# Performance work log

Hardware: AMD Instinct MI355X
Metric: run time of the kernel (lower is better)

The kernel has to match this reference:

```python
import jax, jax.numpy as jnp
import numpy as np

INPUT_DIM = 128
HIDDEN_DIM = 256
TOP_K = 512
M = 8192
N = 8192


def setup_inputs() -> dict:
    key = jax.random.key(0)
    ks = jax.random.split(key, 10)
    s_in = 1.0 / np.sqrt(INPUT_DIM)
    s_h = 1.0 / np.sqrt(HIDDEN_DIM)
    return {
        "desc0": jax.random.normal(ks[0], (1, M, INPUT_DIM), jnp.float32),
        "desc1": jax.random.normal(ks[1], (1, N, INPUT_DIM), jnp.float32),
        # mlpc0: Linear(in,h) -> ReLU -> Linear(h,h); weights stored [in,out]
        "W0a": jax.random.uniform(ks[2], (INPUT_DIM, HIDDEN_DIM), jnp.float32, -s_in, s_in),
        "b0a": jax.random.uniform(ks[3], (HIDDEN_DIM,), jnp.float32, -s_in, s_in),
        "W0b": jax.random.uniform(ks[4], (HIDDEN_DIM, HIDDEN_DIM), jnp.float32, -s_h, s_h),
        "b0b": jax.random.uniform(ks[5], (HIDDEN_DIM,), jnp.float32, -s_h, s_h),
        "W1a": jax.random.uniform(ks[6], (INPUT_DIM, HIDDEN_DIM), jnp.float32, -s_in, s_in),
        "b1a": jax.random.uniform(ks[7], (HIDDEN_DIM,), jnp.float32, -s_in, s_in),
        "W1b": jax.random.uniform(ks[8], (HIDDEN_DIM, HIDDEN_DIM), jnp.float32, -s_h, s_h),
        "b1b": jax.random.uniform(ks[9], (HIDDEN_DIM,), jnp.float32, -s_h, s_h),
    }


def _mlp(x, Wa, ba, Wb, bb):
    h = jax.nn.relu(x @ Wa + ba)
    return h @ Wb + bb


def reference(desc0, desc1, W0a, b0a, W0b, b0b, W1a, b1a, W1b, b1b):
    mdesc0 = _mlp(desc0, W0a, b0a, W0b, b0b)  # [1, M, H]
    mdesc1 = _mlp(desc1, W1a, b1a, W1b, b1b)  # [1, N, H]
    sim = jnp.einsum("bmd,bnd->bmn", mdesc0, mdesc1)  # [1, M, N]
    flat = sim[0].reshape(-1)
    _, top_idx = jax.lax.top_k(flat, TOP_K)
    n = sim.shape[2]
    rows = top_idx // n
    cols = top_idx % n
    top_k_indices_2d = jnp.stack([rows, cols], axis=1)  # [TOP_K, 2]
    return top_k_indices_2d, sim
```

## Files before the change

### kernel.cpp

```cpp
#include <hip/hip_runtime.h>
#include <stdint.h>

#define H_DIM 256
#define NCOL 8192
#define TOPK 512
#define CAND_CAP 8192

typedef unsigned short u16;
typedef __attribute__((ext_vector_type(8))) __bf16 bf16x8;
typedef __attribute__((ext_vector_type(4))) float f32x4;
typedef unsigned __attribute__((address_space(3))) lds_u32;
typedef const unsigned __attribute__((address_space(1))) glb_u32;

__device__ __forceinline__ unsigned fkey(float f) {
  unsigned u = __float_as_uint(f);
  unsigned m = (unsigned)((int)u >> 31) | 0x80000000u;
  return u ^ m;
}

__device__ __forceinline__ u16 f2bf_rne(float f) {
  unsigned u = __float_as_uint(f);
  return (u16)((u + 0x7fffu + ((u >> 16) & 1u)) >> 16);
}

__device__ __forceinline__ float bf2f(u16 h) {
  return __uint_as_float(((unsigned)h) << 16);
}

__global__ __launch_bounds__(256) void mlp_fused(
    const float* __restrict__ X0, const float* __restrict__ W0a,
    const float* __restrict__ b0a, const float* __restrict__ W0b,
    const float* __restrict__ b0b, float* __restrict__ Y0,
    u16* __restrict__ h0, u16* __restrict__ l0,
    const float* __restrict__ X1, const float* __restrict__ W1a,
    const float* __restrict__ b1a, const float* __restrict__ W1b,
    const float* __restrict__ b1b, float* __restrict__ Y1,
    u16* __restrict__ h1, u16* __restrict__ l1,
    unsigned* __restrict__ ghist, unsigned* __restrict__ counter) {
  __shared__ float Xs[16 * 128];
  __shared__ float Hs[16 * 256];
  const int t = threadIdx.x;
  if (blockIdx.x == 0) {
    for (int i = t; i < 4096; i += 256) ghist[i] = 0;
    if (t == 0) *counter = 0;
  }
  const int half = blockIdx.x >> 9;
  const float* X = half ? X1 : X0;
  const float* Wa = half ? W1a : W0a;
  const float* ba = half ? b1a : b0a;
  const float* Wb = half ? W1b : W0b;
  const float* bb_ = half ? b1b : b0b;
  float* Y = half ? Y1 : Y0;
  u16* hi = half ? h1 : h0;
  u16* lo = half ? l1 : l0;
  const int row0 = (blockIdx.x & 511) * 16;

  for (int f = t; f < 512; f += 256) {
    *(float4*)(Xs + f * 4) = *(const float4*)(X + (size_t)row0 * 128 + f * 4);
  }
  __syncthreads();
  const int cg = (t & 63) * 4;
  const int rg = (t >> 6) * 4;

  {
    float acc[4][4];
#pragma unroll
    for (int r = 0; r < 4; r++)
#pragma unroll
      for (int c = 0; c < 4; c++) acc[r][c] = 0.f;
    for (int d = 0; d < 128; d += 4) {
      float4 w0 = *(const float4*)(Wa + (d + 0) * H_DIM + cg);
      float4 w1 = *(const float4*)(Wa + (d + 1) * H_DIM + cg);
      float4 w2 = *(const float4*)(Wa + (d + 2) * H_DIM + cg);
      float4 w3 = *(const float4*)(Wa + (d + 3) * H_DIM + cg);
#pragma unroll
      for (int r = 0; r < 4; r++) {
        float4 x = *(const float4*)(Xs + (rg + r) * 128 + d);
#pragma unroll
        for (int c = 0; c < 4; c++) {
          float a = acc[r][c];
          a = fmaf(x.x, ((const float*)&w0)[c], a);
          a = fmaf(x.y, ((const float*)&w1)[c], a);
          a = fmaf(x.z, ((const float*)&w2)[c], a);
          a = fmaf(x.w, ((const float*)&w3)[c], a);
          acc[r][c] = a;
        }
      }
    }
    const float4 bv = *(const float4*)(ba + cg);
#pragma unroll
    for (int r = 0; r < 4; r++) {
      float4 v;
      v.x = fmaxf(acc[r][0] + bv.x, 0.f);
      v.y = fmaxf(acc[r][1] + bv.y, 0.f);
      v.z = fmaxf(acc[r][2] + bv.z, 0.f);
      v.w = fmaxf(acc[r][3] + bv.w, 0.f);
      *(float4*)(Hs + (rg + r) * 256 + cg) = v;
    }
  }
  __syncthreads();

  {
    float acc[4][4];
#pragma unroll
    for (int r = 0; r < 4; r++)
#pragma unroll
      for (int c = 0; c < 4; c++) acc[r][c] = 0.f;
    for (int d = 0; d < 256; d += 4) {
      float4 w0 = *(const float4*)(Wb + (d + 0) * H_DIM + cg);
      float4 w1 = *(const float4*)(Wb + (d + 1) * H_DIM + cg);
      float4 w2 = *(const float4*)(Wb + (d + 2) * H_DIM + cg);
      float4 w3 = *(const float4*)(Wb + (d + 3) * H_DIM + cg);
#pragma unroll
      for (int r = 0; r < 4; r++) {
        float4 x = *(const float4*)(Hs + (rg + r) * 256 + d);
#pragma unroll
        for (int c = 0; c < 4; c++) {
          float a = acc[r][c];
          a = fmaf(x.x, ((const float*)&w0)[c], a);
          a = fmaf(x.y, ((const float*)&w1)[c], a);
          a = fmaf(x.z, ((const float*)&w2)[c], a);
          a = fmaf(x.w, ((const float*)&w3)[c], a);
          acc[r][c] = a;
        }
      }
    }
    const float4 bv = *(const float4*)(bb_ + cg);
#pragma unroll
    for (int r = 0; r < 4; r++) {
      float4 v;
      v.x = acc[r][0] + bv.x;
      v.y = acc[r][1] + bv.y;
      v.z = acc[r][2] + bv.z;
      v.w = acc[r][3] + bv.w;
      const size_t grow = (size_t)(row0 + rg + r);
      *(float4*)(Y + grow * H_DIM + cg) = v;
      ushort4 hv, lv;
      hv.x = f2bf_rne(v.x); lv.x = f2bf_rne(v.x - bf2f(hv.x));
      hv.y = f2bf_rne(v.y); lv.y = f2bf_rne(v.y - bf2f(hv.y));
      hv.z = f2bf_rne(v.z); lv.z = f2bf_rne(v.z - bf2f(hv.z));
      hv.w = f2bf_rne(v.w); lv.w = f2bf_rne(v.w - bf2f(hv.w));
      *(ushort4*)(hi + grow * H_DIM + cg) = hv;
      *(ushort4*)(lo + grow * H_DIM + cg) = lv;
    }
  }
}

__global__ __launch_bounds__(512, 2) void gemm_sim_mfma(const u16* __restrict__ Ah,
                                                        const u16* __restrict__ Al,
                                                        const u16* __restrict__ Bh,
                                                        const u16* __restrict__ Bl,
                                                        float* __restrict__ C,
                                                        unsigned* __restrict__ ghist) {
  __shared__ __align__(16) char SB[131072];
  const int t = threadIdx.x;
  const int wave = t >> 6, lane = t & 63;
  const int wm = wave >> 2, wn = wave & 3;
  const int bid = blockIdx.x;
  const int swz = (bid & 7) * 128 + (bid >> 3);
  const int m0 = (swz >> 5) * 256, n0 = (swz & 31) * 256;

  f32x4 acc[8][4];
#pragma unroll
  for (int i = 0; i < 8; i++)
#pragma unroll
    for (int j = 0; j < 4; j++) acc[i][j] = (f32x4){0.f, 0.f, 0.f, 0.f};

  const int srow8 = t >> 3;
  const int sA = (t & 7) ^ (srow8 & 7);
  const u16* pAsrc = (sA < 4) ? Ah : Al;
  const u16* pBsrc = (sA < 4) ? Bh : Bl;
  const int scolE = (sA & 3) * 8;
  const int lrow = lane & 15;
  const int kq16 = (lane >> 4) << 4;
  const int asz = (lrow & 7) << 4;
  const int cH = kq16 ^ asz;
  const int cL = (64 + kq16) ^ asz;

  auto STAGE = [&](int bsel, int tt) {
    const int kofs = tt * 32;
    char* base = SB + bsel * 65536;
    const size_t ar = (size_t)(m0 + srow8) * H_DIM + kofs + scolE;
    const size_t br = (size_t)(n0 + srow8) * H_DIM + kofs + scolE;
#pragma unroll
    for (int i = 0; i < 4; i++)
      __builtin_amdgcn_global_load_lds((glb_u32*)(pAsrc + ar + (size_t)i * 64 * H_DIM),
                                       (lds_u32*)(base + i * 8192 + wave * 1024), 16, 0, 0);
#pragma unroll
    for (int i = 0; i < 4; i++)
      __builtin_amdgcn_global_load_lds((glb_u32*)(pBsrc + br + (size_t)i * 64 * H_DIM),
                                       (lds_u32*)(base + 32768 + i * 8192 + wave * 1024), 16, 0, 0);
  };

  STAGE(0, 0);
  for (int tt = 0; tt < 8; ++tt) {
    if (tt < 7) {
      STAGE((tt + 1) & 1, tt + 1);
      asm volatile("s_waitcnt vmcnt(8)" ::: "memory");
    } else {
      asm volatile("s_waitcnt vmcnt(0)" ::: "memory");
    }
    __builtin_amdgcn_s_barrier();
    asm volatile("" ::: "memory");
    const char* bb = SB + (tt & 1) * 65536;
    const char* bA = bb + (wm * 128 + lrow) * 128;
    const char* bB = bb + 32768 + (wn * 64 + lrow) * 128;

    bf16x8 aH[8], bH[4];
#pragma unroll
    for (int fm = 0; fm < 8; fm++) aH[fm] = *(const bf16x8*)(bA + fm * 2048 + cH);
#pragma unroll
    for (int fn = 0; fn < 4; fn++) bH[fn] = *(const bf16x8*)(bB + fn * 2048 + cH);
    __builtin_amdgcn_s_setprio(1);
#pragma unroll
    for (int fm = 0; fm < 8; fm++)
#pragma unroll
      for (int fn = 0; fn < 4; fn++)
        acc[fm][fn] = __builtin_amdgcn_mfma_f32_16x16x32_bf16(aH[fm], bH[fn], acc[fm][fn], 0, 0, 0);
    __builtin_amdgcn_s_setprio(0);
    __builtin_amdgcn_s_barrier();

    {
      bf16x8 bL[4];
#pragma unroll
      for (int fn = 0; fn < 4; fn++) bL[fn] = *(const bf16x8*)(bB + fn * 2048 + cL);
      __builtin_amdgcn_s_setprio(1);
#pragma unroll
      for (int fm = 0; fm < 8; fm++)
#pragma unroll
        for (int fn = 0; fn < 4; fn++)
          acc[fm][fn] = __builtin_amdgcn_mfma_f32_16x16x32_bf16(aH[fm], bL[fn], acc[fm][fn], 0, 0, 0);
      __builtin_amdgcn_s_setprio(0);
    }
    __builtin_amdgcn_s_barrier();

    {
      bf16x8 aL[8];
#pragma unroll
      for (int fm = 0; fm < 8; fm++) aL[fm] = *(const bf16x8*)(bA + fm * 2048 + cL);
      __builtin_amdgcn_s_setprio(1);
#pragma unroll
      for (int fm = 0; fm < 8; fm++)
#pragma unroll
        for (int fn = 0; fn < 4; fn++)
          acc[fm][fn] = __builtin_amdgcn_mfma_f32_16x16x32_bf16(aL[fm], bH[fn], acc[fm][fn], 0, 0, 0);
      __builtin_amdgcn_s_setprio(0);
    }
    __builtin_amdgcn_s_barrier();
    asm volatile("" ::: "memory");
  }

  unsigned* hist = (unsigned*)SB;
  float* Ct = (float*)(SB + 16384);
  for (int i = t; i < 4096; i += 512) hist[i] = 0;
  __syncthreads();
#pragma unroll
  for (int ch = 0; ch < 4; ++ch) {
    if (wm == (ch >> 1)) {
      const int fmb = (ch & 1) * 4;
#pragma unroll
      for (int fi = 0; fi < 4; fi++)
#pragma unroll
        for (int fn = 0; fn < 4; fn++)
#pragma unroll
          for (int q = 0; q < 4; q++)
            Ct[(fi * 16 + (lane >> 4) * 4 + q) * 260 + wn * 64 + fn * 16 + lrow] =
                acc[fmb + fi][fn][q];
    }
    __syncthreads();
#pragma unroll
    for (int u = 0; u < 8; ++u) {
      const int idx = t + u * 512;
      const int row = idx >> 6, c4 = idx & 63;
      float4 v = *(const float4*)(Ct + row * 260 + c4 * 4);
      *(float4*)(C + (size_t)(m0 + ch * 64 + row) * NCOL + n0 + c4 * 4) = v;
      atomicAdd(&hist[fkey(v.x) >> 20], 1u);
      atomicAdd(&hist[fkey(v.y) >> 20], 1u);
      atomicAdd(&hist[fkey(v.z) >> 20], 1u);
      atomicAdd(&hist[fkey(v.w) >> 20], 1u);
    }
    __syncthreads();
  }
  for (int bq = t; bq < 4096; bq += 512) {
    unsigned cc = hist[bq];
    if (cc) atomicAdd(&ghist[bq], cc);
  }
}

__device__ __forceinline__ void cand_push(unsigned kapprox, unsigned thr_m, unsigned idx,
                                          const float* __restrict__ m0f,
                                          const float* __restrict__ m1f,
                                          unsigned long long* __restrict__ cand,
                                          unsigned* __restrict__ counter) {
  if (kapprox >= thr_m) {
    const unsigned row = idx >> 13;
    const unsigned col = idx & 8191u;
    const float4* a4 = (const float4*)(m0f + (size_t)row * H_DIM);
    const float4* b4 = (const float4*)(m1f + (size_t)col * H_DIM);
    float v = 0.f;
#pragma unroll 8
    for (int k = 0; k < H_DIM / 4; k++) {
      float4 a = a4[k], b = b4[k];
      v = fmaf(a.x, b.x, v);
      v = fmaf(a.y, b.y, v);
      v = fmaf(a.z, b.z, v);
      v = fmaf(a.w, b.w, v);
    }
    unsigned p = atomicAdd(counter, 1u);
    if (p < CAND_CAP)
      cand[p] = ((unsigned long long)fkey(v) << 32) |
                (unsigned long long)(0xFFFFFFFFu - idx);
  }
}

__global__ __launch_bounds__(256) void collect(const float* __restrict__ sim,
                                               const unsigned* __restrict__ ghist,
                                               const float* __restrict__ m0f,
                                               const float* __restrict__ m1f,
                                               unsigned long long* __restrict__ cand,
                                               unsigned* __restrict__ counter) {
  __shared__ unsigned part[256];
  __shared__ unsigned thr_sh;
  const int t = threadIdx.x;
  {
    unsigned s = 0;
#pragma unroll
    for (int b = 0; b < 16; b++) s += ghist[t * 16 + b];
    part[t] = s;
    __syncthreads();
    for (int off = 1; off < 256; off <<= 1) {
      unsigned v = part[t] + ((t + off < 256) ? part[t + off] : 0u);
      __syncthreads();
      part[t] = v;
      __syncthreads();
    }
    if (part[t] >= TOPK && (t == 255 || part[t + 1] < TOPK)) {
      unsigned cum = (t == 255) ? 0u : part[t + 1];
      int bsel = t * 16;
      for (int b = t * 16 + 15; b >= t * 16; --b) {
        cum += ghist[b];
        if (cum >= TOPK) { bsel = b; break; }
      }
      thr_sh = (unsigned)bsel << 20;
    }
    __syncthreads();
  }
  const unsigned thr = thr_sh;
  const unsigned thr_m = thr > 4096u ? thr - 4096u : 0u;
  const int stride = gridDim.x * blockDim.x;
  const int total4 = (NCOL * NCOL) / 4;
  const float4* s4 = (const float4*)sim;
  for (int i = blockIdx.x * blockDim.x + threadIdx.x; i < total4; i += stride) {
    float4 v = s4[i];
    unsigned base = (unsigned)i * 4u;
    cand_push(fkey(v.x), thr_m, base + 0u, m0f, m1f, cand, counter);
    cand_push(fkey(v.y), thr_m, base + 1u, m0f, m1f, cand, counter);
    cand_push(fkey(v.z), thr_m, base + 2u, m0f, m1f, cand, counter);
    cand_push(fkey(v.w), thr_m, base + 3u, m0f, m1f, cand, counter);
  }
}

__global__ __launch_bounds__(1024) void sort_topk(const unsigned long long* __restrict__ cand,
                                                  const unsigned* __restrict__ counter,
                                                  float* __restrict__ out) {
  __shared__ unsigned long long top[TOPK];
  __shared__ unsigned wred[16];
  __shared__ unsigned long long pfx_sh;
  __shared__ unsigned cnt_sh;
  const int t = threadIdx.x;
  const int n = (int)min(*counter, (unsigned)CAND_CAP);
  unsigned long long e[CAND_CAP / 1024];
#pragma unroll
  for (int u = 0; u < CAND_CAP / 1024; ++u) {
    const int i = t + u * 1024;
    e[u] = (i < n) ? cand[i] : 0ULL;
  }
  if (t == 0) cnt_sh = 0;
  __syncthreads();
  unsigned long long pfx = 0;
  for (int b = 63; b >= 0; --b) {
    const unsigned long long q = pfx | (1ULL << b);
    unsigned c = 0;
#pragma unroll
    for (int u = 0; u < CAND_CAP / 1024; ++u) c += (e[u] >= q) ? 1u : 0u;
#pragma unroll
    for (int off = 32; off; off >>= 1) c += __shfl_down(c, off, 64);
    if ((t & 63) == 0) wred[t >> 6] = c;
    __syncthreads();
    if (t == 0) {
      unsigned tot = 0;
#pragma unroll
      for (int w = 0; w < 16; ++w) tot += wred[w];
      pfx_sh = (tot >= TOPK) ? q : pfx;
    }
    __syncthreads();
    pfx = pfx_sh;
  }
#pragma unroll
  for (int u = 0; u < CAND_CAP / 1024; ++u) {
    if (e[u] >= pfx) {
      unsigned p = atomicAdd(&cnt_sh, 1u);
      if (p < TOPK) top[p] = e[u];
    }
  }
  __syncthreads();
  for (int k = 2; k <= TOPK; k <<= 1) {
    for (int j = k >> 1; j > 0; j >>= 1) {
      if (t < TOPK) {
        const int l = t ^ j;
        if (l > t) {
          const bool desc = ((t & k) == 0);
          unsigned long long a = top[t], b2 = top[l];
          if (desc ? (a < b2) : (a > b2)) { top[t] = b2; top[l] = a; }
        }
      }
      __syncthreads();
    }
  }
  if (t < TOPK) {
    const unsigned idx = 0xFFFFFFFFu - (unsigned)(top[t] & 0xFFFFFFFFull);
    out[t * 2 + 0] = (float)(idx >> 13);
    out[t * 2 + 1] = (float)(idx & 8191u);
  }
}

extern "C" void kernel_launch(void* const* d_in, const int* in_sizes, int n_in,
                              void* d_out, int out_size, void* d_ws, size_t ws_size,
                              hipStream_t stream) {
  const float* desc0 = (const float*)d_in[0];
  const float* desc1 = (const float*)d_in[1];
  const float* W0a = (const float*)d_in[2];
  const float* b0a = (const float*)d_in[3];
  const float* W0b = (const float*)d_in[4];
  const float* b0b = (const float*)d_in[5];
  const float* W1a = (const float*)d_in[6];
  const float* b1a = (const float*)d_in[7];
  const float* W1b = (const float*)d_in[8];
  const float* b1b = (const float*)d_in[9];

  char* ws = (char*)d_ws;
  unsigned* ghist = (unsigned*)ws;
  unsigned* counter = (unsigned*)(ws + 16384);
  unsigned long long* cand = (unsigned long long*)(ws + 16448);
  float* mdesc0f = (float*)(ws + 131072);
  float* mdesc1f = mdesc0f + 8192 * 256;
  u16* Ahh = (u16*)(mdesc1f + 8192 * 256);
  u16* All = Ahh + 8192 * 256;
  u16* Bhh = All + 8192 * 256;
  u16* Bll = Bhh + 8192 * 256;

  float* outf = (float*)d_out;
  float* sim = outf + TOPK * 2;

  mlp_fused<<<1024, 256, 0, stream>>>(
      desc0, W0a, b0a, W0b, b0b, mdesc0f, Ahh, All,
      desc1, W1a, b1a, W1b, b1b, mdesc1f, Bhh, Bll, ghist, counter);

  gemm_sim_mfma<<<1024, 512, 0, stream>>>(Ahh, All, Bhh, Bll, sim, ghist);
  collect<<<4096, 256, 0, stream>>>(sim, ghist, mdesc0f, mdesc1f, cand, counter);
  sort_topk<<<1, 1024, 0, stream>>>(cand, counter, outf);
}
```

Before: 544.9 us.

## Record per-64x64 tile maxima in GEMM and rescan only qualifying tiles

The GEMM epilogue now reduces each wave's 64x64 sub-tile to a max key and writes it to a tile-max table. The collect step is split into a single-block scan that computes the histogram threshold and builds a worklist of tiles whose max passes it, plus a gather kernel that re-reads only those tiles from sim. This avoids re-reading the full 256 MB similarity matrix just to find candidates. It adds a small serial kernel launch, some extra reduction work in the GEMM epilogue, and a worklist whose size depends on the data.

```diff
diff --git a/kernel.cpp b/kernel.cpp
--- a/kernel.cpp
+++ b/kernel.cpp
@@ -36,13 +36,14 @@
     const float* __restrict__ b1a, const float* __restrict__ W1b,
     const float* __restrict__ b1b, float* __restrict__ Y1,
     u16* __restrict__ h1, u16* __restrict__ l1,
-    unsigned* __restrict__ ghist, unsigned* __restrict__ counter) {
+    unsigned* __restrict__ ghist, unsigned* __restrict__ counter,
+    unsigned* __restrict__ nwork) {
   __shared__ float Xs[16 * 128];
   __shared__ float Hs[16 * 256];
   const int t = threadIdx.x;
   if (blockIdx.x == 0) {
     for (int i = t; i < 4096; i += 256) ghist[i] = 0;
-    if (t == 0) *counter = 0;
+    if (t == 0) { *counter = 0; *nwork = 0; }
   }
   const int half = blockIdx.x >> 9;
   const float* X = half ? X1 : X0;
@@ -151,7 +152,8 @@
                                                         const u16* __restrict__ Bh,
                                                         const u16* __restrict__ Bl,
                                                         float* __restrict__ C,
-                                                        unsigned* __restrict__ ghist) {
+                                                        unsigned* __restrict__ ghist,
+                                                        unsigned* __restrict__ tilemax) {
   __shared__ __align__(16) char SB[131072];
   const int t = threadIdx.x;
   const int wave = t >> 6, lane = t & 63;
@@ -250,6 +252,29 @@
     asm volatile("" ::: "memory");
   }
 
+  {
+    float mx0 = -3.4e38f, mx1 = -3.4e38f;
+#pragma unroll
+    for (int fm = 0; fm < 4; fm++)
+#pragma unroll
+      for (int fn = 0; fn < 4; fn++)
+#pragma unroll
+        for (int q = 0; q < 4; q++) {
+          mx0 = fmaxf(mx0, acc[fm][fn][q]);
+          mx1 = fmaxf(mx1, acc[fm + 4][fn][q]);
+        }
+#pragma unroll
+    for (int off = 1; off < 64; off <<= 1) {
+      mx0 = fmaxf(mx0, __shfl_xor(mx0, off, 64));
+      mx1 = fmaxf(mx1, __shfl_xor(mx1, off, 64));
+    }
+    if (lane == 0) {
+      const int str = (m0 >> 6) + wm * 2, stc = (n0 >> 6) + wn;
+      tilemax[str * 128 + stc] = fkey(mx0);
+      tilemax[(str + 1) * 128 + stc] = fkey(mx1);
+    }
+  }
+
   unsigned* hist = (unsigned*)SB;
   float* Ct = (float*)(SB + 16384);
   for (int i = t; i < 4096; i += 512) hist[i] = 0;
@@ -284,6 +309,46 @@
   for (int bq = t; bq < 4096; bq += 512) {
     unsigned cc = hist[bq];
     if (cc) atomicAdd(&ghist[bq], cc);
+  }
+}
+
+__global__ __launch_bounds__(256) void collect_scan(const unsigned* __restrict__ ghist,
+                                                    const unsigned* __restrict__ tilemax,
+                                                    unsigned* __restrict__ thrm_out,
+                                                    int* __restrict__ worklist,
+                                                    unsigned* __restrict__ nwork) {
+  __shared__ unsigned part[256];
+  __shared__ unsigned thr_sh;
+  const int t = threadIdx.x;
+  unsigned s = 0;
+#pragma unroll
+  for (int b = 0; b < 16; b++) s += ghist[t * 16 + b];
+  part[t] = s;
+  __syncthreads();
+  for (int off = 1; off < 256; off <<= 1) {
+    unsigned v = part[t] + ((t + off < 256) ? part[t + off] : 0u);
+    __syncthreads();
+    part[t] = v;
+    __syncthreads();
+  }
+  if (part[t] >= TOPK && (t == 255 || part[t + 1] < TOPK)) {
+    unsigned cum = (t == 255) ? 0u : part[t + 1];
+    int bsel = t * 16;
+    for (int b = t * 16 + 15; b >= t * 16; --b) {
+      cum += ghist[b];
+      if (cum >= TOPK) { bsel = b; break; }
+    }
+    thr_sh = (unsigned)bsel << 20;
+  }
+  __syncthreads();
+  const unsigned thr = thr_sh;
+  const unsigned thr_m = thr > 4096u ? thr - 4096u : 0u;
+  if (t == 0) *thrm_out = thr_m;
+  for (int i = t; i < 16384; i += 256) {
+    if (tilemax[i] >= thr_m) {
+      unsigned p = atomicAdd(nwork, 1u);
+      worklist[p] = i;
+    }
   }
 }
 
@@ -313,50 +378,32 @@
   }
 }
 
-__global__ __launch_bounds__(256) void collect(const float* __restrict__ sim,
-                                               const unsigned* __restrict__ ghist,
-                                               const float* __restrict__ m0f,
-                                               const float* __restrict__ m1f,
-                                               unsigned long long* __restrict__ cand,
-                                               unsigned* __restrict__ counter) {
-  __shared__ unsigned part[256];
-  __shared__ unsigned thr_sh;
+__global__ __launch_bounds__(256) void collect_gather(const float* __restrict__ sim,
+                                                      const unsigned* __restrict__ thrm_p,
+                                                      const int* __restrict__ worklist,
+                                                      const unsigned* __restrict__ nwork,
+                                                      const float* __restrict__ m0f,
+                                                      const float* __restrict__ m1f,
+                                                      unsigned long long* __restrict__ cand,
+                                                      unsigned* __restrict__ counter) {
+  const unsigned thr_m = *thrm_p;
+  const int nw = (int)*nwork;
   const int t = threadIdx.x;
-  {
-    unsigned s = 0;
-#pragma unroll
-    for (int b = 0; b < 16; b++) s += ghist[t * 16 + b];
-    part[t] = s;
-    __syncthreads();
-    for (int off = 1; off < 256; off <<= 1) {
-      unsigned v = part[t] + ((t + off < 256) ? part[t + off] : 0u);
-      __syncthreads();
-      part[t] = v;
-      __syncthreads();
-    }
-    if (part[t] >= TOPK && (t == 255 || part[t + 1] < TOPK)) {
-      unsigned cum = (t == 255) ? 0u : part[t + 1];
-      int bsel = t * 16;
-      for (int b = t * 16 + 15; b >= t * 16; --b) {
-        cum += ghist[b];
-        if (cum >= TOPK) { bsel = b; break; }
-      }
-      thr_sh = (unsigned)bsel << 20;
-    }
-    __syncthreads();
-  }
-  const unsigned thr = thr_sh;
-  const unsigned thr_m = thr > 4096u ? thr - 4096u : 0u;
-  const int stride = gridDim.x * blockDim.x;
-  const int total4 = (NCOL * NCOL) / 4;
-  const float4* s4 = (const float4*)sim;
-  for (int i = blockIdx.x * blockDim.x + threadIdx.x; i < total4; i += stride) {
-    float4 v = s4[i];
-    unsigned base = (unsigned)i * 4u;
-    cand_push(fkey(v.x), thr_m, base + 0u, m0f, m1f, cand, counter);
-    cand_push(fkey(v.y), thr_m, base + 1u, m0f, m1f, cand, counter);
-    cand_push(fkey(v.z), thr_m, base + 2u, m0f, m1f, cand, counter);
-    cand_push(fkey(v.w), thr_m, base + 3u, m0f, m1f, cand, counter);
+  for (int w = blockIdx.x; w < nw; w += gridDim.x) {
+    const int sid = worklist[w];
+    const int r0 = (sid >> 7) << 6, c0 = (sid & 127) << 6;
+    const float4* base = (const float4*)(sim + (size_t)r0 * NCOL + c0);
+#pragma unroll
+    for (int u = 0; u < 4; ++u) {
+      const int f = t + u * 256;
+      const int row = f >> 4, q4 = f & 15;
+      float4 v = base[(size_t)row * (NCOL / 4) + q4];
+      const unsigned gidx = (unsigned)(r0 + row) * NCOL + c0 + q4 * 4;
+      cand_push(fkey(v.x), thr_m, gidx + 0u, m0f, m1f, cand, counter);
+      cand_push(fkey(v.y), thr_m, gidx + 1u, m0f, m1f, cand, counter);
+      cand_push(fkey(v.z), thr_m, gidx + 2u, m0f, m1f, cand, counter);
+      cand_push(fkey(v.w), thr_m, gidx + 3u, m0f, m1f, cand, counter);
+    }
   }
 }
 
@@ -441,8 +488,12 @@
   char* ws = (char*)d_ws;
   unsigned* ghist = (unsigned*)ws;
   unsigned* counter = (unsigned*)(ws + 16384);
+  unsigned* thrm = (unsigned*)(ws + 16388);
+  unsigned* nwork = (unsigned*)(ws + 16392);
   unsigned long long* cand = (unsigned long long*)(ws + 16448);
-  float* mdesc0f = (float*)(ws + 131072);
+  unsigned* tilemax = (unsigned*)(ws + 98304);
+  int* worklist = (int*)(ws + 163840);
+  float* mdesc0f = (float*)(ws + 262144);
   float* mdesc1f = mdesc0f + 8192 * 256;
   u16* Ahh = (u16*)(mdesc1f + 8192 * 256);
   u16* All = Ahh + 8192 * 256;
@@ -454,9 +505,11 @@
 
   mlp_fused<<<1024, 256, 0, stream>>>(
       desc0, W0a, b0a, W0b, b0b, mdesc0f, Ahh, All,
-      desc1, W1a, b1a, W1b, b1b, mdesc1f, Bhh, Bll, ghist, counter);
-
-  gemm_sim_mfma<<<1024, 512, 0, stream>>>(Ahh, All, Bhh, Bll, sim, ghist);
-  collect<<<4096, 256, 0, stream>>>(sim, ghist, mdesc0f, mdesc1f, cand, counter);
+      desc1, W1a, b1a, W1b, b1b, mdesc1f, Bhh, Bll, ghist, counter, nwork);
+
+  gemm_sim_mfma<<<1024, 512, 0, stream>>>(Ahh, All, Bhh, Bll, sim, ghist, tilemax);
+  collect_scan<<<1, 256, 0, stream>>>(ghist, tilemax, thrm, worklist, nwork);
+  collect_gather<<<1024, 256, 0, stream>>>(sim, thrm, worklist, nwork, mdesc0f, mdesc1f,
+                                           cand, counter);
   sort_topk<<<1, 1024, 0, stream>>>(cand, counter, outf);
 }
```

New measurement: 552.6 us. Within noise of the previous version (+1.4%).
